# Performance work log

Hardware: AMD Instinct MI355X
Metric: run time of the kernel (lower is better)

## Reference

```python
import jax, jax.numpy as jnp
import numpy as np

N = 20000
E = 320000
NEG_SLOPE = 0.2
BN_EPS = 1e-5


def _segment_softmax(e, dst, n):
    # e: [E, H] attention logits, dst: [E] destination node ids
    m = jax.ops.segment_max(e, dst, num_segments=n)           # [N, H]
    ex = jnp.exp(e - m[dst])                                   # [E, H]
    s = jax.ops.segment_sum(ex, dst, num_segments=n)          # [N, H]
    return ex / s[dst]


def gat_conv(x, src, dst, W, a_src, a_dst, b, heads, out_ch):
    # PyG GATConv (concat=True): h = x @ W reshaped to [N, H, C]
    n = x.shape[0]
    h = (x @ W).reshape(n, heads, out_ch)                      # [N, H, C]
    al_s = jnp.einsum('nhc,hc->nh', h, a_src)                  # [N, H]
    al_d = jnp.einsum('nhc,hc->nh', h, a_dst)
    e = jax.nn.leaky_relu(al_s[src] + al_d[dst], NEG_SLOPE)    # [E, H]
    alpha = _segment_softmax(e, dst, n)                        # [E, H]
    msg = h[src] * alpha[:, :, None]                           # [E, H, C]
    out = jax.ops.segment_sum(msg, dst, num_segments=n)        # [N, H, C]
    return out.reshape(n, heads * out_ch) + b


def batch_norm(x, gamma, beta):
    mu = jnp.mean(x, axis=0)
    var = jnp.mean((x - mu) ** 2, axis=0)  # biased, as torch BN training
    return gamma * (x - mu) * jax.lax.rsqrt(var + BN_EPS) + beta


def setup_inputs() -> dict:
    key = jax.random.key(0)
    ks = jax.random.split(key, 16)
    F_in, H1, C1 = 128, 8, 64
    D = H1 * C1  # 512
    OUT = 2
    def gl(k, shape, fan):
        return jax.random.normal(k, shape, dtype=jnp.float32) / np.sqrt(fan)
    x = jax.random.normal(ks[0], (N, F_in), dtype=jnp.float32)
    edge_index = jax.random.randint(ks[1], (2, E), 0, N, dtype=jnp.int64)
    return {
        'x': x, 'edge_index': edge_index,
        'W1': gl(ks[2], (F_in, H1 * C1), F_in),
        'a1s': gl(ks[3], (H1, C1), C1), 'a1d': gl(ks[4], (H1, C1), C1),
        'b1': jnp.zeros((D,), jnp.float32),
        'W2': gl(ks[5], (D, D), D),
        'a2s': gl(ks[6], (1, D), D), 'a2d': gl(ks[7], (1, D), D),
        'b2': jnp.zeros((D,), jnp.float32),
        'fc1_w': gl(ks[8], (D, D), D), 'fc1_b': jnp.zeros((D,), jnp.float32),
        'g1': jnp.ones((D,), jnp.float32), 'be1': jnp.zeros((D,), jnp.float32),
        'fc2_w': gl(ks[9], (D, D), D), 'fc2_b': jnp.zeros((D,), jnp.float32),
        'g2': jnp.ones((D,), jnp.float32), 'be2': jnp.zeros((D,), jnp.float32),
        'lin_w': gl(ks[10], (D, OUT), D), 'lin_b': jnp.zeros((OUT,), jnp.float32),
    }


def reference(x, edge_index, W1, a1s, a1d, b1, W2, a2s, a2d, b2,
              fc1_w, fc1_b, g1, be1, fc2_w, fc2_b, g2, be2, lin_w, lin_b):
    n = x.shape[0]
    loop = jnp.arange(n, dtype=edge_index.dtype)
    src = jnp.concatenate([edge_index[0], loop])  # add self-loops (PyG default)
    dst = jnp.concatenate([edge_index[1], loop])
    h = gat_conv(x, src, dst, W1, a1s, a1d, b1, heads=8, out_ch=64)
    h = batch_norm(jax.nn.relu(h @ fc1_w + fc1_b), g1, be1)
    h = gat_conv(h, src, dst, W2, a2s, a2d, b2, heads=1, out_ch=512)
    h = batch_norm(jax.nn.relu(h @ fc2_w + fc2_b), g2, be2)
    out = jax.nn.relu(h @ lin_w + lin_b)  # dropout p=0 is identity
    return out
```

## Files before the change

### kernel.cpp

```cpp
#include <hip/hip_runtime.h>
#include <hip/hip_bf16.h>

static constexpr int NN = 20000;
static constexpr int EE = 320000;
static constexpr int ET = EE + NN;
static constexpr int DD = 512;
static constexpr int FIN = 128;

typedef __attribute__((ext_vector_type(8))) short short8;
typedef __attribute__((ext_vector_type(4))) float f32x4;

__device__ __forceinline__ unsigned short f2bf(float f) {
    unsigned u = __float_as_uint(f);
    u += 0x7fffu + ((u >> 16) & 1u);
    return (unsigned short)(u >> 16);
}
__device__ __forceinline__ float bf2f(unsigned short b) {
    return __uint_as_float(((unsigned)b) << 16);
}

__device__ __forceinline__ void async_copy16(short* lds, const unsigned short* g) {
    __builtin_amdgcn_global_load_lds(
        (const __attribute__((address_space(1))) unsigned int*)g,
        (__attribute__((address_space(3))) unsigned int*)lds,
        16, 0, 0);
}

__global__ void init_k(int* __restrict__ deg, int* __restrict__ cursor,
                       const unsigned* __restrict__ ei, int* __restrict__ flag) {
    int i = blockIdx.x * blockDim.x + threadIdx.x;
    if (i < NN) { deg[i] = 1; cursor[i] = 0; }
    if (i == 0) {
        int is64 = 1;
        for (int j = 0; j < 64; ++j)
            if (ei[2 * j + 1] != 0u) { is64 = 0; break; }
        *flag = is64;
    }
}

__global__ void count_deg(const void* __restrict__ ei, const int* __restrict__ flag,
                          int* __restrict__ deg) {
    int i = blockIdx.x * blockDim.x + threadIdx.x;
    if (i >= EE) return;
    int d = (*flag) ? (int)((const long long*)ei)[EE + i] : ((const int*)ei)[EE + i];
    atomicAdd(&deg[d], 1);
}

__global__ void scan_k(const int* __restrict__ deg, int* __restrict__ row_ptr) {
    __shared__ int part[1024];
    int t = threadIdx.x;
    const int CH = (NN + 1023) / 1024;
    int start = t * CH;
    int end = min(start + CH, NN);
    int s = 0;
    for (int i = start; i < end; ++i) s += deg[i];
    part[t] = s;
    __syncthreads();
    for (int off = 1; off < 1024; off <<= 1) {
        int v = 0;
        if (t >= off) v = part[t - off];
        __syncthreads();
        part[t] += v;
        __syncthreads();
    }
    int base = (t == 0) ? 0 : part[t - 1];
    for (int i = start; i < end; ++i) { row_ptr[i] = base; base += deg[i]; }
    if (t == 1023) row_ptr[NN] = part[1023];
}

__global__ void fill_csr(const void* __restrict__ ei, const int* __restrict__ flag,
                         const int* __restrict__ row_ptr, int* __restrict__ cursor,
                         int* __restrict__ csr_src) {
    int e = blockIdx.x * blockDim.x + threadIdx.x;
    if (e >= ET) return;
    int s, d;
    if (e < EE) {
        if (*flag) {
            const long long* p = (const long long*)ei;
            s = (int)p[e]; d = (int)p[EE + e];
        } else {
            const int* p = (const int*)ei;
            s = p[e]; d = p[EE + e];
        }
    } else {
        s = d = e - EE;
    }
    int pos = atomicAdd(&cursor[d], 1);
    csr_src[row_ptr[d] + pos] = s;
}

static constexpr int TBLK = 208;
static constexpr int SZ_X = NN * FIN;
static constexpr int SZ_Z = 2 * 1024 + 2 * NN;
__global__ __launch_bounds__(256) void prep_all_k(
    const float* __restrict__ x, const float* __restrict__ W1,
    const float* __restrict__ fc1, const float* __restrict__ W2,
    const float* __restrict__ fc2,
    unsigned short* __restrict__ xb, unsigned short* __restrict__ W1t,
    unsigned short* __restrict__ fc1t, unsigned short* __restrict__ W2t,
    unsigned short* __restrict__ fc2t,
    float* __restrict__ bnstatA, float* __restrict__ bnstatB,
    float* __restrict__ al_s2, float* __restrict__ al_d2) {
    int b = blockIdx.x;
    if (b < TBLK) {
        __shared__ unsigned short tile[64][65];
        const float* src; unsigned short* dst; int rows, cols;
        if (b < 16)       { src = W1;  dst = W1t;  rows = FIN; cols = DD; }
        else if (b < 80)  { b -= 16;  src = fc1; dst = fc1t; rows = DD; cols = DD; }
        else if (b < 144) { b -= 80;  src = W2;  dst = W2t;  rows = DD; cols = DD; }
        else              { b -= 144; src = fc2; dst = fc2t; rows = DD; cols = DD; }
        int tc = cols / 64;
        int r0 = (b / tc) * 64, c0 = (b % tc) * 64;
        int t = threadIdx.x, lr = t >> 6, lc = t & 63;
#pragma unroll
        for (int p = 0; p < 16; ++p) {
            int r = lr + p * 4;
            tile[r][lc] = f2bf(src[(size_t)(r0 + r) * cols + c0 + lc]);
        }
        __syncthreads();
#pragma unroll
        for (int p = 0; p < 16; ++p) {
            int r = lr + p * 4;
            dst[(size_t)(c0 + r) * rows + r0 + lc] = tile[lc][r];
        }
        return;
    }
    int i = (b - TBLK) * 256 + threadIdx.x;
    if (i < SZ_X) { xb[i] = f2bf(x[i]); return; }
    i -= SZ_X;
    if (i < 1024) { bnstatA[i] = 0.f; return; }
    i -= 1024;
    if (i < 1024) { bnstatB[i] = 0.f; return; }
    i -= 1024;
    if (i < NN) { al_s2[i] = 0.f; return; }
    i -= NN;
    if (i < NN) { al_d2[i] = 0.f; return; }
}

template <int RELU, int HASBIAS, int STATS, int ALS, int H>
__global__ __launch_bounds__(256) void gemm_bf16(const unsigned short* __restrict__ A,
                                                 const unsigned short* __restrict__ Bt,
                                                 const float* __restrict__ bias,
                                                 unsigned short* __restrict__ Cb,
                                                 float* __restrict__ bnstat,
                                                 const float* __restrict__ avs,
                                                 const float* __restrict__ avd,
                                                 float* __restrict__ al_s,
                                                 float* __restrict__ al_d,
                                                 int M, int Nc, int K) {
    int id = blockIdx.x;
    int bm = ((id >> 5) << 3) + (id & 7);
    int bn = (id >> 3) & 3;
    int m0 = bm * 128, n0 = bn * 128;
    if (m0 >= M) return;

    __shared__ short As0[128 * 32], As1[128 * 32];
    __shared__ short Bs0[128 * 32], Bs1[128 * 32];
    int t = threadIdx.x;
    int lane = t & 63, w = t >> 6;
    int wm = w & 1, wn = w >> 1;
    int quad = lane >> 4, mr = lane & 15;
    int lrow = lane >> 2;
    int lcol = (lane & 3) * 8;

    const unsigned short* Ag0 = A + (size_t)(m0 + w * 32 + lrow) * K + lcol;
    const unsigned short* Ag1 = A + (size_t)(m0 + w * 32 + 16 + lrow) * K + lcol;
    const unsigned short* Bg0 = Bt + (size_t)(n0 + w * 32 + lrow) * K + lcol;
    const unsigned short* Bg1 = Bt + (size_t)(n0 + w * 32 + 16 + lrow) * K + lcol;
    short* Al[2][2] = {{&As0[(w * 32) * 32], &As0[(w * 32 + 16) * 32]},
                       {&As1[(w * 32) * 32], &As1[(w * 32 + 16) * 32]}};
    short* Bl[2][2] = {{&Bs0[(w * 32) * 32], &Bs0[(w * 32 + 16) * 32]},
                       {&Bs1[(w * 32) * 32], &Bs1[(w * 32 + 16) * 32]}};

    f32x4 zero = {0.f, 0.f, 0.f, 0.f};
    f32x4 acc[4][4];
#pragma unroll
    for (int i = 0; i < 4; ++i)
#pragma unroll
        for (int j = 0; j < 4; ++j) acc[i][j] = zero;

    for (int k0 = 0; k0 < K; k0 += 64) {
        async_copy16(Al[0][0], Ag0 + k0);
        async_copy16(Al[1][0], Ag0 + k0 + 32);
        async_copy16(Al[0][1], Ag1 + k0);
        async_copy16(Al[1][1], Ag1 + k0 + 32);
        async_copy16(Bl[0][0], Bg0 + k0);
        async_copy16(Bl[1][0], Bg0 + k0 + 32);
        async_copy16(Bl[0][1], Bg1 + k0);
        async_copy16(Bl[1][1], Bg1 + k0 + 32);
        __syncthreads();
#pragma unroll
        for (int kp = 0; kp < 2; ++kp) {
            const short* Sa = kp ? As1 : As0;
            const short* Sb = kp ? Bs1 : Bs0;
            short8 af[4], bfr[4];
#pragma unroll
            for (int i = 0; i < 4; ++i) {
                af[i]  = *(const short8*)(&Sa[(wm * 64 + i * 16 + mr) * 32 + quad * 8]);
                bfr[i] = *(const short8*)(&Sb[(wn * 64 + i * 16 + mr) * 32 + quad * 8]);
            }
#pragma unroll
            for (int i = 0; i < 4; ++i)
#pragma unroll
                for (int j = 0; j < 4; ++j)
                    acc[i][j] = __builtin_amdgcn_mfma_f32_16x16x32_bf16(af[i], bfr[j], acc[i][j], 0, 0, 0);
        }
        __syncthreads();
    }

    float as_j[4], ad_j[4];
    if (ALS) {
#pragma unroll
        for (int j = 0; j < 4; ++j) {
            int n = n0 + wn * 64 + j * 16 + mr;
            as_j[j] = avs[n];
            ad_j[j] = avd[n];
        }
    }
    const int head = (H == 8) ? ((n0 + wn * 64) >> 6) : 0;
    float sj[4] = {0.f, 0.f, 0.f, 0.f}, qj[4] = {0.f, 0.f, 0.f, 0.f};
#pragma unroll
    for (int i = 0; i < 4; ++i) {
        int mb = m0 + wm * 64 + i * 16 + quad * 4;
#pragma unroll
        for (int r = 0; r < 4; ++r) {
            int m = mb + r;
            bool valid = (m < M);
            float ps = 0.f, pd = 0.f;
#pragma unroll
            for (int j = 0; j < 4; ++j) {
                int n = n0 + wn * 64 + j * 16 + mr;
                float v = acc[i][j][r];
                if (HASBIAS) v += bias[n];
                if (RELU) v = fmaxf(v, 0.f);
                unsigned short hb = f2bf(v);
                if (valid) Cb[(size_t)m * Nc + n] = hb;
                if (ALS) {
                    float vv = bf2f(hb);
                    ps += as_j[j] * vv;
                    pd += ad_j[j] * vv;
                }
                if (STATS && valid) { sj[j] += v; qj[j] += v * v; }
            }
            if (ALS) {
                ps += __shfl_xor(ps, 1); pd += __shfl_xor(pd, 1);
                ps += __shfl_xor(ps, 2); pd += __shfl_xor(pd, 2);
                ps += __shfl_xor(ps, 4); pd += __shfl_xor(pd, 4);
                ps += __shfl_xor(ps, 8); pd += __shfl_xor(pd, 8);
                if (mr == 0 && valid) {
                    if (H == 8) { al_s[m * 8 + head] = ps; al_d[m * 8 + head] = pd; }
                    else        { atomicAdd(&al_s[m], ps); atomicAdd(&al_d[m], pd); }
                }
            }
        }
    }
    if (STATS) {
#pragma unroll
        for (int j = 0; j < 4; ++j) {
            float s = sj[j], q = qj[j];
            s += __shfl_xor(s, 16); q += __shfl_xor(q, 16);
            s += __shfl_xor(s, 32); q += __shfl_xor(q, 32);
            if (lane < 16) {
                int n = n0 + wn * 64 + j * 16 + mr;
                atomicAdd(&bnstat[n], s);
                atomicAdd(&bnstat[512 + n], q);
            }
        }
    }
}

template <int H>
__global__ __launch_bounds__(256) void gat_gather_k(const unsigned short* __restrict__ hb,
                                                    const float* __restrict__ al_s,
                                                    const float* __restrict__ al_d,
                                                    const int* __restrict__ row_ptr,
                                                    const int* __restrict__ csr_src,
                                                    const float* __restrict__ bias,
                                                    unsigned short* __restrict__ outb) {
    int t = threadIdx.x;
    int w = t >> 6, lane = t & 63;
    int n = blockIdx.x * 4 + w;
    int beg = row_ptr[n], end = row_ptr[n + 1];
    const int hh = (H == 8) ? (lane >> 3) : 0;
    float ald = al_d[n * H + hh];
    float psum = 0.f;
    float acc[8] = {0.f, 0.f, 0.f, 0.f, 0.f, 0.f, 0.f, 0.f};

    for (int p0 = beg; p0 < end; p0 += 64) {
        int cnt = min(64, end - p0);
        int sv = (p0 + lane < end) ? csr_src[p0 + lane] : 0;
        int p = 0;
        for (; p + 8 <= cnt; p += 8) {
            int sn[8];
#pragma unroll
            for (int u = 0; u < 8; ++u) sn[u] = __shfl(sv, p + u);
            float l[8];
#pragma unroll
            for (int u = 0; u < 8; ++u) l[u] = al_s[sn[u] * H + hh] + ald;
            short8 hv[8];
#pragma unroll
            for (int u = 0; u < 8; ++u)
                hv[u] = *(const short8*)(hb + (size_t)sn[u] * DD + lane * 8);
            float a[8];
#pragma unroll
            for (int u = 0; u < 8; ++u) {
                float xx = l[u];
                a[u] = __expf((xx > 0.f) ? xx : 0.2f * xx);
                psum += a[u];
            }
#pragma unroll
            for (int u = 0; u < 8; ++u)
#pragma unroll
                for (int j = 0; j < 8; ++j) acc[j] += a[u] * bf2f((unsigned short)hv[u][j]);
        }
        for (; p < cnt; ++p) {
            int sn0 = __shfl(sv, p);
            float l0 = al_s[sn0 * H + hh] + ald;
            short8 h0 = *(const short8*)(hb + (size_t)sn0 * DD + lane * 8);
            float a0 = __expf((l0 > 0.f) ? l0 : 0.2f * l0);
            psum += a0;
#pragma unroll
            for (int j = 0; j < 8; ++j) acc[j] += a0 * bf2f((unsigned short)h0[j]);
        }
    }
    float inv = 1.0f / psum;
    unsigned short ov[8];
#pragma unroll
    for (int j = 0; j < 8; ++j) ov[j] = f2bf(acc[j] * inv + bias[lane * 8 + j]);
    *(int4*)(outb + (size_t)n * DD + lane * 8) = *(const int4*)ov;
}

__global__ __launch_bounds__(256) void fold1_k(const float* __restrict__ stat,
                                               const float* __restrict__ g,
                                               const float* __restrict__ be,
                                               unsigned short* __restrict__ W2t,
                                               float* __restrict__ bias2) {
    int t = threadIdx.x;
    int n = blockIdx.x * 4 + (t >> 6);
    int lane = t & 63;
    float pb = 0.f;
#pragma unroll
    for (int j = 0; j < 8; ++j) {
        int k = lane * 8 + j;
        float mean = stat[k] * (1.0f / NN);
        float var = stat[512 + k] * (1.0f / NN) - mean * mean;
        float sc = g[k] * rsqrtf(var + 1e-5f);
        float sh = be[k] - mean * sc;
        float wv = bf2f(W2t[n * DD + k]);
        W2t[n * DD + k] = f2bf(sc * wv);
        pb += sh * wv;
    }
    for (int off = 32; off; off >>= 1) pb += __shfl_down(pb, off);
    if (lane == 0) bias2[n] = pb;
}

__global__ void final_linear(const unsigned short* __restrict__ xb,
                             const float* __restrict__ stat, const float* __restrict__ g,
                             const float* __restrict__ be, const float* __restrict__ w,
                             const float* __restrict__ b, float* __restrict__ out) {
    int wave = (blockIdx.x * blockDim.x + threadIdx.x) >> 6;
    int lane = threadIdx.x & 63;
    if (wave >= NN) return;
    short8 hv = *(const short8*)(xb + (size_t)wave * DD + lane * 8);
    float p0 = 0.f, p1 = 0.f;
#pragma unroll
    for (int j = 0; j < 8; ++j) {
        int c = lane * 8 + j;
        float mean = stat[c] * (1.0f / NN);
        float var = stat[512 + c] * (1.0f / NN) - mean * mean;
        float sc = g[c] * rsqrtf(var + 1e-5f);
        float vn = (bf2f((unsigned short)hv[j]) - mean) * sc + be[c];
        p0 += vn * w[2 * c];
        p1 += vn * w[2 * c + 1];
    }
    for (int off = 32; off; off >>= 1) {
        p0 += __shfl_down(p0, off);
        p1 += __shfl_down(p1, off);
    }
    if (lane == 0) {
        out[wave * 2 + 0] = fmaxf(p0 + b[0], 0.f);
        out[wave * 2 + 1] = fmaxf(p1 + b[1], 0.f);
    }
}

extern "C" void kernel_launch(void* const* d_in, const int* in_sizes, int n_in,
                              void* d_out, int out_size, void* d_ws, size_t ws_size,
                              hipStream_t stream) {
    const float* x     = (const float*)d_in[0];
    const void*  ei    = d_in[1];
    const float* W1    = (const float*)d_in[2];
    const float* a1s   = (const float*)d_in[3];
    const float* a1d   = (const float*)d_in[4];
    const float* b1    = (const float*)d_in[5];
    const float* W2    = (const float*)d_in[6];
    const float* a2s   = (const float*)d_in[7];
    const float* a2d   = (const float*)d_in[8];
    const float* b2    = (const float*)d_in[9];
    const float* fc1_w = (const float*)d_in[10];
    const float* fc1_b = (const float*)d_in[11];
    const float* g1    = (const float*)d_in[12];
    const float* be1   = (const float*)d_in[13];
    const float* fc2_w = (const float*)d_in[14];
    const float* fc2_b = (const float*)d_in[15];
    const float* g2    = (const float*)d_in[16];
    const float* be2   = (const float*)d_in[17];
    const float* lin_w = (const float*)d_in[18];
    const float* lin_b = (const float*)d_in[19];
    float* out = (float*)d_out;

    char* ws = (char*)d_ws;
    auto alloc = [&](size_t bytes) {
        void* p = (void*)ws;
        ws += (bytes + 255) & ~size_t(255);
        return p;
    };
    unsigned short* h_bf    = (unsigned short*)alloc((size_t)NN * DD * 2);
    unsigned short* act_bf  = (unsigned short*)alloc((size_t)NN * DD * 2);
    unsigned short* W1t     = (unsigned short*)alloc((size_t)DD * FIN * 2);
    unsigned short* fc1t    = (unsigned short*)alloc((size_t)DD * DD * 2);
    unsigned short* W2t     = (unsigned short*)alloc((size_t)DD * DD * 2);
    unsigned short* fc2t    = (unsigned short*)alloc((size_t)DD * DD * 2);
    float*          al_s    = (float*)alloc((size_t)NN * 8 * 4);
    float*          al_d    = (float*)alloc((size_t)NN * 8 * 4);
    float*          al_s2   = (float*)alloc((size_t)NN * 4);
    float*          al_d2   = (float*)alloc((size_t)NN * 4);
    int*            row_ptr = (int*)alloc((size_t)(NN + 1) * 4);
    int*            deg     = (int*)alloc((size_t)NN * 4);
    int*            cursor  = (int*)alloc((size_t)NN * 4);
    int*            csr_src = (int*)alloc((size_t)ET * 4);
    int*            flag    = (int*)alloc(256);
    float*          bnstatA = (float*)alloc(1024 * 4);
    float*          bnstatB = (float*)alloc(1024 * 4);
    float*          bias2f  = (float*)alloc(512 * 4);

    init_k<<<(NN + 255) / 256, 256, 0, stream>>>(deg, cursor, (const unsigned*)ei, flag);
    count_deg<<<(EE + 255) / 256, 256, 0, stream>>>(ei, flag, deg);
    scan_k<<<1, 1024, 0, stream>>>(deg, row_ptr);
    fill_csr<<<(ET + 255) / 256, 256, 0, stream>>>(ei, flag, row_ptr, cursor, csr_src);

    unsigned short* x_bf = act_bf;
    const int prep_blocks = TBLK + (SZ_X + SZ_Z + 255) / 256;
    prep_all_k<<<prep_blocks, 256, 0, stream>>>(x, W1, fc1_w, W2, fc2_w,
                                                x_bf, W1t, fc1t, W2t, fc2t,
                                                bnstatA, bnstatB, al_s2, al_d2);

    const int GB = 640;

    gemm_bf16<0, 0, 0, 1, 8><<<GB, 256, 0, stream>>>(
        x_bf, W1t, nullptr, h_bf, nullptr, a1s, a1d, al_s, al_d, NN, DD, FIN);
    gat_gather_k<8><<<NN / 4, 256, 0, stream>>>(h_bf, al_s, al_d, row_ptr, csr_src, b1, act_bf);
    gemm_bf16<1, 1, 1, 0, 8><<<GB, 256, 0, stream>>>(
        act_bf, fc1t, fc1_b, h_bf, bnstatA, nullptr, nullptr, nullptr, nullptr, NN, DD, DD);
    fold1_k<<<128, 256, 0, stream>>>(bnstatA, g1, be1, W2t, bias2f);

    gemm_bf16<0, 1, 0, 1, 1><<<GB, 256, 0, stream>>>(
        h_bf, W2t, bias2f, act_bf, nullptr, a2s, a2d, al_s2, al_d2, NN, DD, DD);
    gat_gather_k<1><<<NN / 4, 256, 0, stream>>>(act_bf, al_s2, al_d2, row_ptr, csr_src, b2, h_bf);
    gemm_bf16<1, 1, 1, 0, 8><<<GB, 256, 0, stream>>>(
        h_bf, fc2t, fc2_b, act_bf, bnstatB, nullptr, nullptr, nullptr, nullptr, NN, DD, DD);

    final_linear<<<(NN + 3) / 4, 256, 0, stream>>>(act_bf, bnstatB, g2, be2, lin_w, lin_b, out);
}
```

Before: 366.9 us.

## Split GAT gather across column slices and replace init kernel with memsets

The gather kernel now splits each destination node's 512 columns into four 128-column slices handled by separate blocks. Each lane loads 4 bytes (two bf16 values) per neighbour instead of 16 bytes, which gives four times as many blocks and fewer registers per thread, at the cost of recomputing the attention weights and reloading the neighbour indices once per slice. Block indices are interleaved so that neighbouring blocks cover the same nodes and can share cache. Index-width detection moves to the host, based on the input buffer size and used as a template parameter. The init kernel and the zeroing tail of the prep kernel are replaced by memsets, and the self-loop degree is added inside the scan.

Result: slower. 383.8 us (+4.6%).

```diff
diff --git a/kernel.cpp b/kernel.cpp
--- a/kernel.cpp
+++ b/kernel.cpp
@@ -26,23 +26,11 @@
         16, 0, 0);
 }
 
-__global__ void init_k(int* __restrict__ deg, int* __restrict__ cursor,
-                       const unsigned* __restrict__ ei, int* __restrict__ flag) {
-    int i = blockIdx.x * blockDim.x + threadIdx.x;
-    if (i < NN) { deg[i] = 1; cursor[i] = 0; }
-    if (i == 0) {
-        int is64 = 1;
-        for (int j = 0; j < 64; ++j)
-            if (ei[2 * j + 1] != 0u) { is64 = 0; break; }
-        *flag = is64;
-    }
-}
-
-__global__ void count_deg(const void* __restrict__ ei, const int* __restrict__ flag,
-                          int* __restrict__ deg) {
+template <int IS64>
+__global__ void count_deg(const void* __restrict__ ei, int* __restrict__ deg) {
     int i = blockIdx.x * blockDim.x + threadIdx.x;
     if (i >= EE) return;
-    int d = (*flag) ? (int)((const long long*)ei)[EE + i] : ((const int*)ei)[EE + i];
+    int d = IS64 ? (int)((const long long*)ei)[EE + i] : ((const int*)ei)[EE + i];
     atomicAdd(&deg[d], 1);
 }
 
@@ -53,7 +41,7 @@
     int start = t * CH;
     int end = min(start + CH, NN);
     int s = 0;
-    for (int i = start; i < end; ++i) s += deg[i];
+    for (int i = start; i < end; ++i) s += deg[i] + 1;
     part[t] = s;
     __syncthreads();
     for (int off = 1; off < 1024; off <<= 1) {
@@ -64,18 +52,19 @@
         __syncthreads();
     }
     int base = (t == 0) ? 0 : part[t - 1];
-    for (int i = start; i < end; ++i) { row_ptr[i] = base; base += deg[i]; }
+    for (int i = start; i < end; ++i) { row_ptr[i] = base; base += deg[i] + 1; }
     if (t == 1023) row_ptr[NN] = part[1023];
 }
 
-__global__ void fill_csr(const void* __restrict__ ei, const int* __restrict__ flag,
+template <int IS64>
+__global__ void fill_csr(const void* __restrict__ ei,
                          const int* __restrict__ row_ptr, int* __restrict__ cursor,
                          int* __restrict__ csr_src) {
     int e = blockIdx.x * blockDim.x + threadIdx.x;
     if (e >= ET) return;
     int s, d;
     if (e < EE) {
-        if (*flag) {
+        if (IS64) {
             const long long* p = (const long long*)ei;
             s = (int)p[e]; d = (int)p[EE + e];
         } else {
@@ -91,16 +80,13 @@
 
 static constexpr int TBLK = 208;
 static constexpr int SZ_X = NN * FIN;
-static constexpr int SZ_Z = 2 * 1024 + 2 * NN;
 __global__ __launch_bounds__(256) void prep_all_k(
     const float* __restrict__ x, const float* __restrict__ W1,
     const float* __restrict__ fc1, const float* __restrict__ W2,
     const float* __restrict__ fc2,
     unsigned short* __restrict__ xb, unsigned short* __restrict__ W1t,
     unsigned short* __restrict__ fc1t, unsigned short* __restrict__ W2t,
-    unsigned short* __restrict__ fc2t,
-    float* __restrict__ bnstatA, float* __restrict__ bnstatB,
-    float* __restrict__ al_s2, float* __restrict__ al_d2) {
+    unsigned short* __restrict__ fc2t) {
     int b = blockIdx.x;
     if (b < TBLK) {
         __shared__ unsigned short tile[64][65];
@@ -126,15 +112,7 @@
         return;
     }
     int i = (b - TBLK) * 256 + threadIdx.x;
-    if (i < SZ_X) { xb[i] = f2bf(x[i]); return; }
-    i -= SZ_X;
-    if (i < 1024) { bnstatA[i] = 0.f; return; }
-    i -= 1024;
-    if (i < 1024) { bnstatB[i] = 0.f; return; }
-    i -= 1024;
-    if (i < NN) { al_s2[i] = 0.f; return; }
-    i -= NN;
-    if (i < NN) { al_d2[i] = 0.f; return; }
+    if (i < SZ_X) xb[i] = f2bf(x[i]);
 }
 
 template <int RELU, int HASBIAS, int STATS, int ALS, int H>
@@ -277,14 +255,18 @@
                                                     const int* __restrict__ csr_src,
                                                     const float* __restrict__ bias,
                                                     unsigned short* __restrict__ outb) {
+    int b = blockIdx.x;
+    int slice = (b & 7) >> 1;
+    int g = ((b >> 3) << 1) | (b & 1);
     int t = threadIdx.x;
     int w = t >> 6, lane = t & 63;
-    int n = blockIdx.x * 4 + w;
+    int n = g * 4 + w;
+    int col = slice * 128 + lane * 2;
+    const int hh = (H == 8) ? (col >> 6) : 0;
+    float ald = al_d[n * H + hh];
     int beg = row_ptr[n], end = row_ptr[n + 1];
-    const int hh = (H == 8) ? (lane >> 3) : 0;
-    float ald = al_d[n * H + hh];
-    float psum = 0.f;
-    float acc[8] = {0.f, 0.f, 0.f, 0.f, 0.f, 0.f, 0.f, 0.f};
+    const char* hbase = (const char*)(hb + col);
+    float acc0 = 0.f, acc1 = 0.f, psum = 0.f;
 
     for (int p0 = beg; p0 < end; p0 += 64) {
         int cnt = min(64, end - p0);
@@ -297,10 +279,10 @@
             float l[8];
 #pragma unroll
             for (int u = 0; u < 8; ++u) l[u] = al_s[sn[u] * H + hh] + ald;
-            short8 hv[8];
+            unsigned hv[8];
 #pragma unroll
             for (int u = 0; u < 8; ++u)
-                hv[u] = *(const short8*)(hb + (size_t)sn[u] * DD + lane * 8);
+                hv[u] = *(const unsigned*)(hbase + ((unsigned)sn[u] << 10));
             float a[8];
 #pragma unroll
             for (int u = 0; u < 8; ++u) {
@@ -309,25 +291,26 @@
                 psum += a[u];
             }
 #pragma unroll
-            for (int u = 0; u < 8; ++u)
-#pragma unroll
-                for (int j = 0; j < 8; ++j) acc[j] += a[u] * bf2f((unsigned short)hv[u][j]);
+            for (int u = 0; u < 8; ++u) {
+                acc0 = fmaf(a[u], __uint_as_float(hv[u] << 16), acc0);
+                acc1 = fmaf(a[u], __uint_as_float(hv[u] & 0xffff0000u), acc1);
+            }
         }
         for (; p < cnt; ++p) {
             int sn0 = __shfl(sv, p);
             float l0 = al_s[sn0 * H + hh] + ald;
-            short8 h0 = *(const short8*)(hb + (size_t)sn0 * DD + lane * 8);
+            unsigned h0 = *(const unsigned*)(hbase + ((unsigned)sn0 << 10));
             float a0 = __expf((l0 > 0.f) ? l0 : 0.2f * l0);
             psum += a0;
-#pragma unroll
-            for (int j = 0; j < 8; ++j) acc[j] += a0 * bf2f((unsigned short)h0[j]);
+            acc0 = fmaf(a0, __uint_as_float(h0 << 16), acc0);
+            acc1 = fmaf(a0, __uint_as_float(h0 & 0xffff0000u), acc1);
         }
     }
     float inv = 1.0f / psum;
-    unsigned short ov[8];
-#pragma unroll
-    for (int j = 0; j < 8; ++j) ov[j] = f2bf(acc[j] * inv + bias[lane * 8 + j]);
-    *(int4*)(outb + (size_t)n * DD + lane * 8) = *(const int4*)ov;
+    float2 bv = *(const float2*)(bias + col);
+    unsigned short o0 = f2bf(acc0 * inv + bv.x);
+    unsigned short o1 = f2bf(acc1 * inv + bv.y);
+    *(unsigned*)(outb + (size_t)n * DD + col) = ((unsigned)o1 << 16) | (unsigned)o0;
 }
 
 __global__ __launch_bounds__(256) void fold1_k(const float* __restrict__ stat,
@@ -428,34 +411,49 @@
     int*            deg     = (int*)alloc((size_t)NN * 4);
     int*            cursor  = (int*)alloc((size_t)NN * 4);
     int*            csr_src = (int*)alloc((size_t)ET * 4);
-    int*            flag    = (int*)alloc(256);
     float*          bnstatA = (float*)alloc(1024 * 4);
     float*          bnstatB = (float*)alloc(1024 * 4);
     float*          bias2f  = (float*)alloc(512 * 4);
 
-    init_k<<<(NN + 255) / 256, 256, 0, stream>>>(deg, cursor, (const unsigned*)ei, flag);
-    count_deg<<<(EE + 255) / 256, 256, 0, stream>>>(ei, flag, deg);
+    const int is64 = (in_sizes[1] >= (int)(2u * EE * 8u)) ? 1 : 0;
+
+    hipMemsetAsync(deg, 0, (size_t)NN * 4, stream);
+    hipMemsetAsync(cursor, 0, (size_t)NN * 4, stream);
+    hipMemsetAsync(bnstatA, 0, 1024 * 4, stream);
+    hipMemsetAsync(bnstatB, 0, 1024 * 4, stream);
+    hipMemsetAsync(al_s2, 0, (size_t)NN * 4, stream);
+    hipMemsetAsync(al_d2, 0, (size_t)NN * 4, stream);
+
+    if (is64) {
+        count_deg<1><<<(EE + 255) / 256, 256, 0, stream>>>(ei, deg);
+    } else {
+        count_deg<0><<<(EE + 255) / 256, 256, 0, stream>>>(ei, deg);
+    }
     scan_k<<<1, 1024, 0, stream>>>(deg, row_ptr);
-    fill_csr<<<(ET + 255) / 256, 256, 0, stream>>>(ei, flag, row_ptr, cursor, csr_src);
+    if (is64) {
+        fill_csr<1><<<(ET + 255) / 256, 256, 0, stream>>>(ei, row_ptr, cursor, csr_src);
+    } else {
+        fill_csr<0><<<(ET + 255) / 256, 256, 0, stream>>>(ei, row_ptr, cursor, csr_src);
+    }
 
     unsigned short* x_bf = act_bf;
-    const int prep_blocks = TBLK + (SZ_X + SZ_Z + 255) / 256;
+    const int prep_blocks = TBLK + (SZ_X + 255) / 256;
     prep_all_k<<<prep_blocks, 256, 0, stream>>>(x, W1, fc1_w, W2, fc2_w,
-                                                x_bf, W1t, fc1t, W2t, fc2t,
-                                                bnstatA, bnstatB, al_s2, al_d2);
+                                                x_bf, W1t, fc1t, W2t, fc2t);
 
     const int GB = 640;
+    const int GGB = NN / 4 * 4;
 
     gemm_bf16<0, 0, 0, 1, 8><<<GB, 256, 0, stream>>>(
         x_bf, W1t, nullptr, h_bf, nullptr, a1s, a1d, al_s, al_d, NN, DD, FIN);
-    gat_gather_k<8><<<NN / 4, 256, 0, stream>>>(h_bf, al_s, al_d, row_ptr, csr_src, b1, act_bf);
+    gat_gather_k<8><<<GGB, 256, 0, stream>>>(h_bf, al_s, al_d, row_ptr, csr_src, b1, act_bf);
     gemm_bf16<1, 1, 1, 0, 8><<<GB, 256, 0, stream>>>(
         act_bf, fc1t, fc1_b, h_bf, bnstatA, nullptr, nullptr, nullptr, nullptr, NN, DD, DD);
     fold1_k<<<128, 256, 0, stream>>>(bnstatA, g1, be1, W2t, bias2f);
 
     gemm_bf16<0, 1, 0, 1, 1><<<GB, 256, 0, stream>>>(
         h_bf, W2t, bias2f, act_bf, nullptr, a2s, a2d, al_s2, al_d2, NN, DD, DD);
-    gat_gather_k<1><<<NN / 4, 256, 0, stream>>>(act_bf, al_s2, al_d2, row_ptr, csr_src, b2, h_bf);
+    gat_gather_k<1><<<GGB, 256, 0, stream>>>(act_bf, al_s2, al_d2, row_ptr, csr_src, b2, h_bf);
     gemm_bf16<1, 1, 1, 0, 8><<<GB, 256, 0, stream>>>(
         h_bf, fc2t, fc2_b, act_bf, bnstatB, nullptr, nullptr, nullptr, nullptr, NN, DD, DD);
 
```
